# Optimization experiments

Hardware: AMD Instinct MI355X
Metric: run time of the kernel (lower is better)

Reference implementation:

```python
import jax, jax.numpy as jnp
import numpy as np

B, N_IN, NV, F = 1, 65536, 1, 64
N_OUT, K = 16384, 16
N_DIST, N_PHI, OUT = 4, 8, 256
DIST_MAX = 0.1  # grid_layers[level_out].min_dist stand-in


def setup_inputs() -> dict:
    key = jax.random.key(0)
    ks = jax.random.split(key, 6)
    x = jax.random.normal(ks[0], (B, N_IN, NV, F), dtype=jnp.float32)
    nh_idx = jax.random.randint(ks[1], (N_OUT, K), 0, N_IN)  # neighbor gather indices
    d_dists = jax.random.uniform(ks[2], (N_OUT, K), dtype=jnp.float32) * DIST_MAX
    d_phi = jax.random.uniform(ks[3], (N_OUT, K), dtype=jnp.float32) * (2 * np.pi) - np.pi
    dists = jnp.linspace(0.0, DIST_MAX, N_DIST, dtype=jnp.float32)          # anchor distances
    sigma = jnp.asarray(DIST_MAX / 2, dtype=jnp.float32)                     # n_sigma == 1 -> scalar
    phi = jnp.linspace(-np.pi, np.pi, N_PHI + 1, dtype=jnp.float32)[:-1]     # von Mises: phi_min = -pi
    kappa = jnp.asarray(1.0, dtype=jnp.float32)                              # kappa_init
    W_out = jax.random.normal(ks[4], (F * N_DIST * N_PHI, OUT), dtype=jnp.float32) / np.sqrt(F * N_DIST * N_PHI)
    return {"x": x, "d_dists": d_dists, "d_phi": d_phi, "dists": dists,
            "sigma": sigma, "kappa": kappa, "phi": phi, "W_out": W_out, "nh_idx": nh_idx}


def reference(x, d_dists, d_phi, dists, sigma, kappa, phi, W_out, nh_idx):
    # Gaussian distance kernel: exp(-0.5*((d - dist_k)/sigma)^2)  -> (N_OUT, K, N_DIST)
    w_d = jnp.exp(-0.5 * ((d_dists[..., None] - dists) / sigma) ** 2)
    # von Mises angular kernel: exp(kappa * cos(d_phi - phi_p))   -> (N_OUT, K, N_PHI)
    w_p = jnp.exp(kappa * jnp.cos(d_phi[..., None] - phi))
    # combined kernel weights, normalized over the K neighbors per anchor
    w = w_d[..., :, None] * w_p[..., None, :]                      # (N_OUT, K, N_DIST, N_PHI)
    w = w / (jnp.sum(w, axis=1, keepdims=True) + 1e-9)
    w = w.reshape(N_OUT, K, N_DIST * N_PHI)                        # (N_OUT, K, M)
    # gather neighbor features from the input grid
    x_nb = x[:, nh_idx]                                            # (B, N_OUT, K, NV, F)
    # weighted aggregation over neighbors -> enhanced channels
    agg = jnp.einsum('bnkvf,nkm->bnvmf', x_nb, w)                  # (B, N_OUT, NV, M, F)
    agg = agg.reshape(B, N_OUT, NV, N_DIST * N_PHI * F)            # model_dim_enhanced = 2048
    return agg @ W_out                                             # (B, N_OUT, NV, OUT)
```

## Files before the change

kernel.cpp:

```cpp
#include <hip/hip_runtime.h>
#include <hip/hip_bf16.h>

#define N_IN   65536
#define N_OUTP 16384
#define KNB    16
#define FDIM   64
#define M_DIM  32
#define KDIM   2048
#define OUT_D  256

typedef __bf16 bf16x8_t __attribute__((ext_vector_type(8)));
typedef float  f32x4_t  __attribute__((ext_vector_type(4)));
typedef float  f32x2_t  __attribute__((ext_vector_type(2)));


__device__ __forceinline__ unsigned pk2(float a, float b) {
  __bf16 b0 = (__bf16)a, b1 = (__bf16)b;
  return ((unsigned)__builtin_bit_cast(unsigned short, b1) << 16) |
          (unsigned)__builtin_bit_cast(unsigned short, b0);
}
__device__ __forceinline__ float ulo(unsigned u) {
  return __builtin_bit_cast(float, u << 16);
}
__device__ __forceinline__ float uhi(unsigned u) {
  return __builtin_bit_cast(float, u & 0xffff0000u);
}

#define WST 580
#define WKS 36
#define XPS 576
#define XPK 36
#define AGG_LDS 36992

__global__ __launch_bounds__(256, 4) void agg_kernel(
    const float* __restrict__ x,
    const float* __restrict__ d_dists,
    const float* __restrict__ d_phi,
    const float* __restrict__ dists,
    const float* __restrict__ sigma_p,
    const float* __restrict__ kappa_p,
    const float* __restrict__ phi,
    const float* __restrict__ W,
    const int*   __restrict__ nh_idx,
    uint4*       __restrict__ Aws,
    uint4*       __restrict__ Bws)
{
  __shared__ __align__(16) char smem_raw[AGG_LDS];
  float*    wbuf = (float*)smem_raw;
  unsigned* xpk  = (unsigned*)(smem_raw + 18560);

  const int t  = threadIdx.x;
  const int n0 = blockIdx.x * 8;
  const int T  = blockIdx.x >> 1;
  const int r0 = (blockIdx.x & 1) * 8;

  const int h = t & 1, gk = (t >> 1) & 15, gr8 = t >> 5;
  const int gidx = nh_idx[(n0 + gr8) * KNB + gk];
  const float4* xr = (const float4*)x + (size_t)gidx * 16 + h * 8;
  float4 xreg[8];
#pragma unroll
  for (int j = 0; j < 8; ++j) xreg[j] = xr[j];

  {
    const float sinv = 1.0f / sigma_p[0];
    const float kap  = kappa_p[0];
    float phiv[8], distv[4];
#pragma unroll
    for (int p = 0; p < 8; ++p) phiv[p] = phi[p];
#pragma unroll
    for (int d = 0; d < 4; ++d) distv[d] = dists[d];

    int rk = t >> 1, r8w = rk >> 4, k = rk & 15, rep = t & 1;
    int n = n0 + r8w;
    float dd = d_dists[n * KNB + k];
    float dp = d_phi[n * KNB + k];
    float wp[8];
#pragma unroll
    for (int p = 0; p < 8; ++p) wp[p] = __expf(kap * __cosf(dp - phiv[p]));
#pragma unroll
    for (int dl = 0; dl < 2; ++dl) {
      int d = rep * 2 + dl;
      float td = (dd - distv[d]) * sinv;
      float wd = __expf(-0.5f * td * td);
      float* dst = wbuf + r8w * WST + k * WKS + d * 8;
      *(float4*)(dst)     = make_float4(wd * wp[0], wd * wp[1], wd * wp[2], wd * wp[3]);
      *(float4*)(dst + 4) = make_float4(wd * wp[4], wd * wp[5], wd * wp[6], wd * wp[7]);
    }
  }

  {
    unsigned u[16];
#pragma unroll
    for (int j = 0; j < 8; ++j) {
      u[2 * j]     = pk2(xreg[j].x, xreg[j].y);
      u[2 * j + 1] = pk2(xreg[j].z, xreg[j].w);
    }
    uint4* xd = (uint4*)(xpk + gr8 * XPS + gk * XPK + h * 16);
#pragma unroll
    for (int q = 0; q < 4; ++q)
      xd[q] = make_uint4(u[4 * q], u[4 * q + 1], u[4 * q + 2], u[4 * q + 3]);
  }
  __syncthreads();

  {
    const int r8 = t & 7, fo = (t >> 3) & 7, mq = t >> 6;
    f32x2_t acc[8][4];
    float   den[8];
#pragma unroll
    for (int mi = 0; mi < 8; ++mi) {
      den[mi] = 0.f;
#pragma unroll
      for (int fj = 0; fj < 4; ++fj) acc[mi][fj] = (f32x2_t){0.f, 0.f};
    }

    const float*    wp_ = wbuf + r8 * WST + mq * 8;
    const unsigned* xp_ = xpk + r8 * XPS + fo * 4;

#pragma unroll 8
    for (int k = 0; k < 16; ++k) {
      float4 wa = *(const float4*)(wp_ + k * WKS);
      float4 wbv = *(const float4*)(wp_ + k * WKS + 4);
      uint4 xu = *(const uint4*)(xp_ + k * XPK);
      float wv[8] = {wa.x, wa.y, wa.z, wa.w, wbv.x, wbv.y, wbv.z, wbv.w};
      f32x2_t xv[4];
      xv[0] = (f32x2_t){ulo(xu.x), uhi(xu.x)};
      xv[1] = (f32x2_t){ulo(xu.y), uhi(xu.y)};
      xv[2] = (f32x2_t){ulo(xu.z), uhi(xu.z)};
      xv[3] = (f32x2_t){ulo(xu.w), uhi(xu.w)};
#pragma unroll
      for (int mi = 0; mi < 8; ++mi) {
        den[mi] += wv[mi];
        f32x2_t wmm = (f32x2_t){wv[mi], wv[mi]};
#pragma unroll
        for (int fj = 0; fj < 4; ++fj)
          acc[mi][fj] += wmm * xv[fj];
      }
    }

    uint4* base = Aws + (size_t)T * 4096 + (fo & 3) * 16 + r0 + r8
                      + (size_t)(fo >> 2) * 64;
#pragma unroll
    for (int mi = 0; mi < 8; ++mi) {
      int m = mq * 8 + mi;
      float wn = 1.0f / (den[mi] + 1e-9f);
      uint4 v;
      v.x = pk2(acc[mi][0][0] * wn, acc[mi][0][1] * wn);
      v.y = pk2(acc[mi][1][0] * wn, acc[mi][1][1] * wn);
      v.z = pk2(acc[mi][2][0] * wn, acc[mi][2][1] * wn);
      v.w = pk2(acc[mi][3][0] * wn, acc[mi][3][1] * wn);
      base[m * 128] = v;
    }
  }

  if (blockIdx.x < 64) {
    __syncthreads();
    float* wlds = (float*)smem_raw;
    const int kk = blockIdx.x;

    const float4* Wb = (const float4*)(W + kk * 32 * OUT_D);
#pragma unroll
    for (int i = 0; i < 8; ++i) {
      int idx = i * 256 + t;
      int row = idx >> 6, c4 = idx & 63;
      float4 v = Wb[idx];
      *(float4*)(wlds + row * 260 + c4 * 4) = v;
    }
    __syncthreads();

#pragma unroll
    for (int j = 0; j < 4; ++j) {
      int c  = j * 256 + t;
      int l  = c & 63, nt = c >> 6;
      int rr = (l >> 4) * 8, col = nt * 16 + (l & 15);
      union { unsigned short s[8]; uint4 v; } u;
#pragma unroll
      for (int jj = 0; jj < 8; ++jj) {
        __bf16 b = (__bf16)wlds[(rr + jj) * 260 + col];
        u.s[jj] = __builtin_bit_cast(unsigned short, b);
      }
      Bws[(size_t)kk * 1024 + c] = u.v;
    }
  }
}

__global__ __launch_bounds__(512, 2) void gemm_kernel(
    const uint4* __restrict__ Astream,
    const uint4* __restrict__ Bws,
    float*       __restrict__ out)
{
  __shared__ float red[4][64 * 68];

  const int t    = threadIdx.x;
  const int lane = t & 63;
  const int w    = t >> 6;
  const int cg   = w & 3;
  const int half = w >> 2;
  const int rb   = blockIdx.x;

  const uint4* pa = Astream + (size_t)(rb * 4) * 4096 + half * 64 + lane;
  const uint4* pb = Bws + (half * 16 + cg * 4) * 64 + lane;

  f32x4_t cacc[4][4];
#pragma unroll
  for (int mt = 0; mt < 4; ++mt)
#pragma unroll
    for (int i = 0; i < 4; ++i)
      cacc[mt][i] = (f32x4_t){0.f, 0.f, 0.f, 0.f};

  uint4 a[4][4], b[4][4];
#pragma unroll
  for (int s = 0; s < 4; ++s) {
#pragma unroll
    for (int mt = 0; mt < 4; ++mt) a[s][mt] = pa[mt * 4096 + s * 128];
#pragma unroll
    for (int i = 0; i < 4; ++i)    b[s][i]  = pb[s * 2048 + i * 64];
  }

#pragma unroll 4
  for (int j = 0; j < 32; ++j) {
    const int s = j & 3;
    bf16x8_t B0 = __builtin_bit_cast(bf16x8_t, b[s][0]);
    bf16x8_t B1 = __builtin_bit_cast(bf16x8_t, b[s][1]);
    bf16x8_t B2 = __builtin_bit_cast(bf16x8_t, b[s][2]);
    bf16x8_t B3 = __builtin_bit_cast(bf16x8_t, b[s][3]);
#pragma unroll
    for (int mt = 0; mt < 4; ++mt) {
      bf16x8_t A = __builtin_bit_cast(bf16x8_t, a[s][mt]);
      cacc[mt][0] = __builtin_amdgcn_mfma_f32_16x16x32_bf16(A, B0, cacc[mt][0], 0, 0, 0);
      cacc[mt][1] = __builtin_amdgcn_mfma_f32_16x16x32_bf16(A, B1, cacc[mt][1], 0, 0, 0);
      cacc[mt][2] = __builtin_amdgcn_mfma_f32_16x16x32_bf16(A, B2, cacc[mt][2], 0, 0, 0);
      cacc[mt][3] = __builtin_amdgcn_mfma_f32_16x16x32_bf16(A, B3, cacc[mt][3], 0, 0, 0);
    }
    if (j < 28) {
#pragma unroll
      for (int mt = 0; mt < 4; ++mt) a[s][mt] = pa[mt * 4096 + (j + 4) * 128];
#pragma unroll
      for (int i = 0; i < 4; ++i)    b[s][i]  = pb[(j + 4) * 2048 + i * 64];
    }
  }

  const int lrow = (lane >> 4) * 4;
  const int lcol = lane & 15;

  if (half == 0) {
#pragma unroll
    for (int mt = 0; mt < 4; ++mt)
#pragma unroll
      for (int i = 0; i < 4; ++i)
#pragma unroll
        for (int reg = 0; reg < 4; ++reg)
          red[cg][(mt * 16 + lrow + reg) * 68 + i * 16 + lcol] = cacc[mt][i][reg];
  }
  __syncthreads();
  if (half == 1) {
#pragma unroll
    for (int mt = 0; mt < 4; ++mt)
#pragma unroll
      for (int i = 0; i < 4; ++i)
#pragma unroll
        for (int reg = 0; reg < 4; ++reg) {
          int row = mt * 16 + lrow + reg;
          int col = i * 16 + lcol;
          float v = red[cg][row * 68 + col] + cacc[mt][i][reg];
          out[(rb * 64 + row) * OUT_D + cg * 64 + col] = v;
        }
  }
}

extern "C" void kernel_launch(void* const* d_in, const int* in_sizes, int n_in,
                              void* d_out, int out_size, void* d_ws, size_t ws_size,
                              hipStream_t stream) {
  const float* x      = (const float*)d_in[0];
  const float* dd     = (const float*)d_in[1];
  const float* dp     = (const float*)d_in[2];
  const float* dists  = (const float*)d_in[3];
  const float* sigma  = (const float*)d_in[4];
  const float* kappa  = (const float*)d_in[5];
  const float* phi    = (const float*)d_in[6];
  const float* W      = (const float*)d_in[7];
  const int*   nh     = (const int*)d_in[8];
  float*       out    = (float*)d_out;

  uint4* Bws = (uint4*)d_ws;
  uint4* Aws = (uint4*)((char*)d_ws + (1 << 20));

  agg_kernel<<<N_OUTP / 8, 256, 0, stream>>>(
      x, dd, dp, dists, sigma, kappa, phi, W, nh, Aws, Bws);
  gemm_kernel<<<N_OUTP / 64, 512, 0, stream>>>(Aws, Bws, out);
}
```

Before: 58.10 us.

## Drop split-K reduction in GEMM; give each wave a full-K 32x64 tile

The GEMM no longer splits K across two wave halves that are then reduced through shared memory. Each of the 8 waves now owns a 32-row by 64-column output tile, runs the full K loop with a 2-deep register prefetch, and writes results straight to global memory. Dropping the LDS reduction buffer and using fewer accumulators allows a launch-bounds occupancy hint of 4 instead of 2. The cost is a longer serial K loop per wave, a shallower prefetch, and less MFMA work per loaded A and B fragment.

```diff
diff --git a/kernel.cpp b/kernel.cpp
--- a/kernel.cpp
+++ b/kernel.cpp
@@ -183,88 +183,63 @@
   }
 }
 
-__global__ __launch_bounds__(512, 2) void gemm_kernel(
+__global__ __launch_bounds__(512, 4) void gemm_kernel(
     const uint4* __restrict__ Astream,
     const uint4* __restrict__ Bws,
     float*       __restrict__ out)
 {
-  __shared__ float red[4][64 * 68];
-
   const int t    = threadIdx.x;
   const int lane = t & 63;
   const int w    = t >> 6;
-  const int cg   = w & 3;
-  const int half = w >> 2;
   const int rb   = blockIdx.x;
 
-  const uint4* pa = Astream + (size_t)(rb * 4) * 4096 + half * 64 + lane;
-  const uint4* pb = Bws + (half * 16 + cg * 4) * 64 + lane;
-
-  f32x4_t cacc[4][4];
-#pragma unroll
-  for (int mt = 0; mt < 4; ++mt)
+  const uint4* pa = Astream + (size_t)(rb * 4 + (w & 1) * 2) * 4096 + lane;
+  const uint4* pb = Bws + ((w >> 1) * 4) * 64 + lane;
+
+  f32x4_t cacc[2][4];
+#pragma unroll
+  for (int mt = 0; mt < 2; ++mt)
 #pragma unroll
     for (int i = 0; i < 4; ++i)
       cacc[mt][i] = (f32x4_t){0.f, 0.f, 0.f, 0.f};
 
-  uint4 a[4][4], b[4][4];
-#pragma unroll
-  for (int s = 0; s < 4; ++s) {
-#pragma unroll
-    for (int mt = 0; mt < 4; ++mt) a[s][mt] = pa[mt * 4096 + s * 128];
-#pragma unroll
-    for (int i = 0; i < 4; ++i)    b[s][i]  = pb[s * 2048 + i * 64];
+  uint4 a[2][2], b[2][4];
+#pragma unroll
+  for (int s = 0; s < 2; ++s) {
+    a[s][0] = pa[s * 64];
+    a[s][1] = pa[4096 + s * 64];
+#pragma unroll
+    for (int i = 0; i < 4; ++i) b[s][i] = pb[s * 1024 + i * 64];
   }
 
 #pragma unroll 4
-  for (int j = 0; j < 32; ++j) {
-    const int s = j & 3;
-    bf16x8_t B0 = __builtin_bit_cast(bf16x8_t, b[s][0]);
-    bf16x8_t B1 = __builtin_bit_cast(bf16x8_t, b[s][1]);
-    bf16x8_t B2 = __builtin_bit_cast(bf16x8_t, b[s][2]);
-    bf16x8_t B3 = __builtin_bit_cast(bf16x8_t, b[s][3]);
-#pragma unroll
-    for (int mt = 0; mt < 4; ++mt) {
-      bf16x8_t A = __builtin_bit_cast(bf16x8_t, a[s][mt]);
-      cacc[mt][0] = __builtin_amdgcn_mfma_f32_16x16x32_bf16(A, B0, cacc[mt][0], 0, 0, 0);
-      cacc[mt][1] = __builtin_amdgcn_mfma_f32_16x16x32_bf16(A, B1, cacc[mt][1], 0, 0, 0);
-      cacc[mt][2] = __builtin_amdgcn_mfma_f32_16x16x32_bf16(A, B2, cacc[mt][2], 0, 0, 0);
-      cacc[mt][3] = __builtin_amdgcn_mfma_f32_16x16x32_bf16(A, B3, cacc[mt][3], 0, 0, 0);
-    }
-    if (j < 28) {
-#pragma unroll
-      for (int mt = 0; mt < 4; ++mt) a[s][mt] = pa[mt * 4096 + (j + 4) * 128];
-#pragma unroll
-      for (int i = 0; i < 4; ++i)    b[s][i]  = pb[(j + 4) * 2048 + i * 64];
-    }
-  }
-
-  const int lrow = (lane >> 4) * 4;
-  const int lcol = lane & 15;
-
-  if (half == 0) {
-#pragma unroll
-    for (int mt = 0; mt < 4; ++mt)
-#pragma unroll
-      for (int i = 0; i < 4; ++i)
-#pragma unroll
-        for (int reg = 0; reg < 4; ++reg)
-          red[cg][(mt * 16 + lrow + reg) * 68 + i * 16 + lcol] = cacc[mt][i][reg];
-  }
-  __syncthreads();
-  if (half == 1) {
-#pragma unroll
-    for (int mt = 0; mt < 4; ++mt)
-#pragma unroll
-      for (int i = 0; i < 4; ++i)
-#pragma unroll
-        for (int reg = 0; reg < 4; ++reg) {
-          int row = mt * 16 + lrow + reg;
-          int col = i * 16 + lcol;
-          float v = red[cg][row * 68 + col] + cacc[mt][i][reg];
-          out[(rb * 64 + row) * OUT_D + cg * 64 + col] = v;
-        }
-  }
+  for (int kk = 0; kk < 64; ++kk) {
+    const int s = kk & 1;
+    bf16x8_t A0 = __builtin_bit_cast(bf16x8_t, a[s][0]);
+    bf16x8_t A1 = __builtin_bit_cast(bf16x8_t, a[s][1]);
+#pragma unroll
+    for (int i = 0; i < 4; ++i) {
+      bf16x8_t B = __builtin_bit_cast(bf16x8_t, b[s][i]);
+      cacc[0][i] = __builtin_amdgcn_mfma_f32_16x16x32_bf16(A0, B, cacc[0][i], 0, 0, 0);
+      cacc[1][i] = __builtin_amdgcn_mfma_f32_16x16x32_bf16(A1, B, cacc[1][i], 0, 0, 0);
+    }
+    if (kk < 62) {
+      a[s][0] = pa[(kk + 2) * 64];
+      a[s][1] = pa[4096 + (kk + 2) * 64];
+#pragma unroll
+      for (int i = 0; i < 4; ++i) b[s][i] = pb[(kk + 2) * 1024 + i * 64];
+    }
+  }
+
+  const int rbase = rb * 64 + (w & 1) * 32 + (lane >> 4) * 4;
+  const int cbase = (w >> 1) * 64 + (lane & 15);
+#pragma unroll
+  for (int mt = 0; mt < 2; ++mt)
+#pragma unroll
+    for (int i = 0; i < 4; ++i)
+#pragma unroll
+      for (int reg = 0; reg < 4; ++reg)
+        out[(rbase + mt * 16 + reg) * OUT_D + cbase + i * 16] = cacc[mt][i][reg];
 }
 
 extern "C" void kernel_launch(void* const* d_in, const int* in_sizes, int n_in,
```

After: 67.27 us. 15.8% more time.
